# Optimization experiments

Hardware: AMD Instinct MI355X
Metric: run time of the kernel (lower is better)

Reference implementation:

```python
import jax, jax.numpy as jnp
import numpy as np

L, B = 256, 512
K, IN, STATE, OBS = 128, 64, 128, 128


def _preprocess(x, w1, b1, w2, b2):
    # PreProcess: two Linear+ReLU layers mapping raw dim -> k
    t = jax.nn.relu(x @ w1.T + b1)
    return jax.nn.relu(t @ w2.T + b2)


def _dblock_relu(x, w1, b1, w2, b2, wmu, bmu, wls, bls):
    # DBlock (TD-VAE style) with ReLU in place of tanh:
    # t = relu(fc1(x)) * sigmoid(fc2(x)); mu = fc_mu(t); logsigma = fc_logsigma(t)
    t = jax.nn.relu(x @ w1.T + b1) * jax.nn.sigmoid(x @ w2.T + b2)
    return t @ wmu.T + bmu, t @ wls.T + bls


def setup_inputs() -> dict:
    key = jax.random.key(0)
    ks = jax.random.split(key, 24)
    rn = lambda i, shape, s=1.0: jax.random.normal(ks[i], shape, dtype=jnp.float32) * s
    W = 0.05  # small weight scale for numerical stability
    return {
        "external_input_seq": rn(0, (L, B, IN)),
        "observations_seq": rn(1, (L, B, OBS)),
        "eps": rn(2, (L, B, STATE)),
        "u_w1": rn(3, (K, IN), W), "u_b1": jnp.zeros((K,), jnp.float32),
        "u_w2": rn(4, (K, K), W), "u_b2": jnp.zeros((K,), jnp.float32),
        "x_w1": rn(5, (K, OBS), W), "x_b1": jnp.zeros((K,), jnp.float32),
        "x_w2": rn(6, (K, K), W), "x_b2": jnp.zeros((K,), jnp.float32),
        "post_w1": rn(7, (2 * K, 2 * K), W), "post_b1": jnp.zeros((2 * K,), jnp.float32),
        "post_w2": rn(8, (2 * K, 2 * K), W), "post_b2": jnp.zeros((2 * K,), jnp.float32),
        "post_wmu": rn(9, (STATE, 2 * K), W), "post_bmu": jnp.zeros((STATE,), jnp.float32),
        "post_wls": rn(10, (STATE, 2 * K), W), "post_bls": jnp.zeros((STATE,), jnp.float32),
        "gru_wih": rn(11, (3 * K, K), W), "gru_whh": rn(12, (3 * K, K), W),
        "gru_bih": jnp.zeros((3 * K,), jnp.float32), "gru_bhh": jnp.zeros((3 * K,), jnp.float32),
    }


def reference(external_input_seq, observations_seq, eps,
              u_w1, u_b1, u_w2, u_b2,
              x_w1, x_b1, x_w2, x_b2,
              post_w1, post_b1, post_w2, post_b2,
              post_wmu, post_bmu, post_wls, post_bls,
              gru_wih, gru_whh, gru_bih, gru_bhh):
    # _forward_posterior of VAERNN (num_layers=1 GRU)
    u_embed = _preprocess(external_input_seq, u_w1, u_b1, u_w2, u_b2)  # (L,B,K)
    x_embed = _preprocess(observations_seq, x_w1, x_b1, x_w2, x_b2)    # (L,B,K)

    # Precompute input-side GRU gates for all timesteps (one big GEMM)
    x_gates = u_embed @ gru_wih.T + gru_bih  # (L,B,3K)

    h0 = jnp.zeros((external_input_seq.shape[1], K), dtype=external_input_seq.dtype)

    def step(h, xg):
        hg = h @ gru_whh.T + gru_bhh
        xr, xz, xn = jnp.split(xg, 3, axis=-1)
        hr, hz, hn_ = jnp.split(hg, 3, axis=-1)
        r = jax.nn.sigmoid(xr + hr)
        z = jax.nn.sigmoid(xz + hz)
        n = jnp.tanh(xn + r * hn_)
        h_new = (1.0 - z) * n + z * h
        return h_new, h  # emit PRE-update hidden (matches h_seq[:-1])

    hn_final, h_seq = jax.lax.scan(step, h0, x_gates)  # h_seq: (L,B,K)

    # Posterior q(z_t | o_t, h_{t-1}) -- fully parallel over time since z_t
    # never feeds back into the recurrence in this model.
    post_in = jnp.concatenate([x_embed, h_seq], axis=-1)  # (L,B,2K)
    state_mu, state_logsigma = _dblock_relu(
        post_in, post_w1, post_b1, post_w2, post_b2,
        post_wmu, post_bmu, post_wls, post_bls)
    # reparameterized sample from N(mu, diag(exp(logsigma)^2))
    sampled_state = state_mu + jnp.exp(state_logsigma) * eps

    return state_mu, state_logsigma, sampled_state, h_seq, x_embed
```

## Files before the change

kernel.cpp:

```cpp
#include <hip/hip_runtime.h>


typedef __attribute__((ext_vector_type(8))) short bf16x8;
typedef __attribute__((ext_vector_type(4))) short bf16x4;
typedef __attribute__((ext_vector_type(4))) float f32x4;

#define LB 131072

__device__ __forceinline__ short f2b(float f) {
  union { float f; unsigned u; } v; v.f = f;
  unsigned r = (v.u + 0x7FFFu + ((v.u >> 16) & 1u)) >> 16;
  return (short)r;
}
__device__ __forceinline__ float u2f(unsigned u) {
  union { unsigned u; float f; } v; v.u = u << 16; return v.f;
}
__device__ __forceinline__ float rcpf(float x) { return __builtin_amdgcn_rcpf(x); }
__device__ __forceinline__ float exp2f_(float x) { return __builtin_amdgcn_exp2f(x); }
__device__ __forceinline__ float sigm(float x) { return rcpf(1.f + exp2f_(-1.44269504f * x)); }

#define LGKM_BAR()                                          \
  asm volatile("s_waitcnt lgkmcnt(0)" ::: "memory");        \
  __builtin_amdgcn_s_barrier();                             \
  __builtin_amdgcn_sched_barrier(0);

__global__ __launch_bounds__(256) void k_cvt(
    const float* __restrict__ s0, const float* __restrict__ s1,
    const float* __restrict__ s2, const float* __restrict__ s3,
    const float* __restrict__ s4, const float* __restrict__ s5,
    const float* __restrict__ s6, const float* __restrict__ s7,
    const float* __restrict__ s8, const float* __restrict__ s9,
    short* __restrict__ dst)
{
  int i = blockIdx.x * 256 + threadIdx.x;
  if (i >= 352256) return;
  const float* src; int off;
  if      (i <   8192) { src = s0; off = i; }
  else if (i <  24576) { src = s1; off = i - 8192; }
  else if (i <  40960) { src = s2; off = i - 24576; }
  else if (i <  57344) { src = s3; off = i - 40960; }
  else if (i < 106496) { src = s4; off = i - 57344; }
  else if (i < 155648) { src = s5; off = i - 106496; }
  else if (i < 221184) { src = s6; off = i - 155648; }
  else if (i < 286720) { src = s7; off = i - 221184; }
  else if (i < 319488) { src = s8; off = i - 286720; }
  else                 { src = s9; off = i - 319488; }
  dst[i] = f2b(src[off]);
}

#define UT 8
__global__ __launch_bounds__(512) void k_upath(
    const float* __restrict__ x, const short* __restrict__ w1, const float* __restrict__ b1,
    const short* __restrict__ w2, const float* __restrict__ b2,
    const short* __restrict__ wih, const float* __restrict__ bih,
    const float* __restrict__ bhh,
    short* __restrict__ gates)
{
  __shared__ short Xb[32][72];
  __shared__ short Tb[32][136];
  __shared__ short Gb[32][392];
  const int tid = threadIdx.x, w = tid >> 6, l = tid & 63;
  const int lr = l & 15, lg = l >> 4;
  const int n1 = w * 16 + lr;

  bf16x8 wf1[2], wf2[4], wfg[3][4];
  #pragma unroll
  for (int kt = 0; kt < 2; ++kt)
    wf1[kt] = *reinterpret_cast<const bf16x8*>(w1 + (size_t)n1 * 64 + kt * 32 + lg * 8);
  #pragma unroll
  for (int kt = 0; kt < 4; ++kt)
    wf2[kt] = *reinterpret_cast<const bf16x8*>(w2 + (size_t)n1 * 128 + kt * 32 + lg * 8);
  float bgv[3];
  #pragma unroll
  for (int j = 0; j < 3; ++j) {
    const int cg = w * 48 + j * 16 + lr;
    bgv[j] = bih[cg] + (cg < 256 ? bhh[cg] : 0.f);
    #pragma unroll
    for (int kt = 0; kt < 4; ++kt)
      wfg[j][kt] = *reinterpret_cast<const bf16x8*>(wih + (size_t)cg * 128 + kt * 32 + lg * 8);
  }
  const float b1v = b1[n1], b2v = b2[n1];
  const int srow = tid >> 4, scol4 = (tid & 15) * 4, gcol = (tid & 15) * 24;

  float4 sx = *reinterpret_cast<const float4*>(
      x + ((size_t)blockIdx.x * UT * 32 + srow) * 64 + scol4);

  for (int it = 0; it < UT; ++it) {
    const size_t m0 = ((size_t)blockIdx.x * UT + it) * 32;

    {
      bf16x4 p; p[0] = f2b(sx.x); p[1] = f2b(sx.y); p[2] = f2b(sx.z); p[3] = f2b(sx.w);
      *reinterpret_cast<bf16x4*>(&Xb[srow][scol4]) = p;
    }
    LGKM_BAR();

    {
      const size_t mn = ((size_t)blockIdx.x * UT + (it + 1 < UT ? it + 1 : it)) * 32;
      sx = *reinterpret_cast<const float4*>(x + (mn + srow) * 64 + scol4);
    }

    f32x4 a1c[2] = {(f32x4){0.f,0.f,0.f,0.f}, (f32x4){0.f,0.f,0.f,0.f}};
    #pragma unroll
    for (int kt = 0; kt < 2; ++kt) {
      #pragma unroll
      for (int mt = 0; mt < 2; ++mt) {
        bf16x8 af = *reinterpret_cast<const bf16x8*>(&Xb[mt * 16 + lr][kt * 32 + lg * 8]);
        a1c[mt] = __builtin_amdgcn_mfma_f32_16x16x32_bf16(af, wf1[kt], a1c[mt], 0, 0, 0);
      }
    }
    #pragma unroll
    for (int mt = 0; mt < 2; ++mt)
      #pragma unroll
      for (int r = 0; r < 4; ++r) {
        float v = a1c[mt][r] + b1v;
        Tb[mt * 16 + lg * 4 + r][n1] = f2b(v > 0.f ? v : 0.f);
      }
    LGKM_BAR();

    f32x4 a2c[2] = {(f32x4){0.f,0.f,0.f,0.f}, (f32x4){0.f,0.f,0.f,0.f}};
    #pragma unroll
    for (int kt = 0; kt < 4; ++kt) {
      #pragma unroll
      for (int mt = 0; mt < 2; ++mt) {
        bf16x8 af = *reinterpret_cast<const bf16x8*>(&Tb[mt * 16 + lr][kt * 32 + lg * 8]);
        a2c[mt] = __builtin_amdgcn_mfma_f32_16x16x32_bf16(af, wf2[kt], a2c[mt], 0, 0, 0);
      }
    }
    #pragma unroll
    for (int mt = 0; mt < 2; ++mt)
      #pragma unroll
      for (int r = 0; r < 4; ++r) {
        float v = a2c[mt][r] + b2v;
        Gb[mt * 16 + lg * 4 + r][n1] = f2b(v > 0.f ? v : 0.f);
      }
    LGKM_BAR();

    bf16x8 ag[2][4];
    #pragma unroll
    for (int mt = 0; mt < 2; ++mt)
      #pragma unroll
      for (int kt = 0; kt < 4; ++kt)
        ag[mt][kt] = *reinterpret_cast<const bf16x8*>(&Gb[mt * 16 + lr][kt * 32 + lg * 8]);
    LGKM_BAR();

    #pragma unroll
    for (int j = 0; j < 3; ++j) {
      #pragma unroll
      for (int mt = 0; mt < 2; ++mt) {
        f32x4 c = {0.f, 0.f, 0.f, 0.f};
        #pragma unroll
        for (int kt = 0; kt < 4; ++kt)
          c = __builtin_amdgcn_mfma_f32_16x16x32_bf16(ag[mt][kt], wfg[j][kt], c, 0, 0, 0);
        #pragma unroll
        for (int r = 0; r < 4; ++r)
          Gb[mt * 16 + lg * 4 + r][w * 48 + j * 16 + lr] = f2b(c[r] + bgv[j]);
      }
    }
    LGKM_BAR();

    #pragma unroll
    for (int k = 0; k < 3; ++k) {
      bf16x8 vv = *reinterpret_cast<const bf16x8*>(&Gb[srow][gcol + k * 8]);
      *reinterpret_cast<bf16x8*>(gates + (m0 + srow) * 384 + gcol + k * 8) = vv;
    }
  }
}

__global__ __launch_bounds__(512) void k_grux(
    const short* __restrict__ gates, const short* __restrict__ whh,
    const float* __restrict__ bhh, float* __restrict__ hseq,
    const float* __restrict__ obs, const short* __restrict__ xw1,
    const float* __restrict__ xb1, const short* __restrict__ xw2,
    const float* __restrict__ xb2, float* __restrict__ xe)
{
  __shared__ short smem_[41088];
  const int tid = threadIdx.x, w = tid >> 6, l = tid & 63;
  const int lr = l & 15, lg = l >> 4;

  if (blockIdx.x < 128) {
    short (*hb)[16][136] = reinterpret_cast<short (*)[16][136]>(smem_);
    const int m0 = blockIdx.x * 4;
    const int c = w * 16 + lr;
    const int row = lg;
    const size_t gr = m0 + row;

    bf16x8 bfr[3][4];
    #pragma unroll
    for (int g = 0; g < 3; ++g)
      #pragma unroll
      for (int kt = 0; kt < 4; ++kt)
        bfr[g][kt] = *reinterpret_cast<const bf16x8*>(whh + (size_t)(g * 128 + c) * 128 + kt * 32 + lg * 8);
    const float bbn = bhh[256 + c];

    for (int i = tid; i < 2 * 16 * 136; i += 512) smem_[i] = 0;

    float hold = 0.f;

    unsigned gA[3], gB[3];
    #pragma unroll
    for (int g = 0; g < 3; ++g) {
      gA[g] = (unsigned short)gates[gr * 384 + g * 128 + c];
      gB[g] = (unsigned short)gates[(512 + gr) * 384 + g * 128 + c];
    }

    __syncthreads();
    __builtin_amdgcn_s_setprio(1);

#define GATE_E(G, OUT)                                                         \
  {                                                                            \
    f32x4 cc = {0.f, 0.f, 0.f, 0.f};                                           \
    _Pragma("unroll")                                                          \
    for (int kt = 0; kt < 4; ++kt)                                             \
      cc = __builtin_amdgcn_mfma_f32_16x16x32_bf16(a_[kt], bfr[G][kt], cc, 0, 0, 0); \
    unsigned u0 = __float_as_uint(cc[0]), u2 = __float_as_uint(cc[2]);         \
    unsigned u1 = __float_as_uint(cc[1]), u3 = __float_as_uint(cc[3]);         \
    asm volatile("v_permlane32_swap_b32 %0, %1" : "+v"(u0), "+v"(u2));         \
    asm volatile("v_permlane32_swap_b32 %0, %1" : "+v"(u1), "+v"(u3));         \
    asm volatile("v_permlane16_swap_b32 %0, %1" : "+v"(u0), "+v"(u1));         \
    OUT = __uint_as_float(u0);                                                 \
  }

#define GRU_STEP(T, GC, BR, BW)                                                \
  {                                                                            \
    const int t_ = (T);                                                        \
    bf16x8 a_[4];                                                              \
    _Pragma("unroll")                                                          \
    for (int kt = 0; kt < 4; ++kt)                                             \
      a_[kt] = *reinterpret_cast<const bf16x8*>(&hb[BR][lr][kt * 32 + lg * 8]);\
    float e0, e1, e2;                                                          \
    GATE_E(0, e0)                            \
    float rr = sigm(u2f(GC[0]) + e0);                                          \
    GATE_E(2, e2)                                           \
    float tt = u2f(GC[2]) + (e2 + bbn) * rr;                                   \
    float nn = 1.f - 2.f * rcpf(1.f + exp2f_(2.88539008f * tt));               \
    GATE_E(1, e1)                         \
    float zz = sigm(u2f(GC[1]) + e1);                                          \
    float hnew = nn + zz * (hold - nn);                                        \
    hb[BW][row][c] = f2b(hnew);           \
    hseq[((size_t)t_ * 512 + gr) * 128 + c] = hold;                            \
    hold = hnew;                                                               \
    const int tp_ = (t_ + 2) & 255;                                            \
    _Pragma("unroll")                                                          \
    for (int g = 0; g < 3; ++g)                                                \
      GC[g] = (unsigned short)gates[((size_t)tp_ * 512 + gr) * 384 + g * 128 + c]; \
    asm volatile("s_waitcnt lgkmcnt(0)" ::: "memory");                         \
    __builtin_amdgcn_s_barrier();                                              \
    __builtin_amdgcn_sched_barrier(0);                                         \
  }

    for (int tt = 0; tt < 128; ++tt) {
      GRU_STEP(2 * tt,     gA, 0, 1)
      GRU_STEP(2 * tt + 1, gB, 1, 0)
    }
    __builtin_amdgcn_s_setprio(0);
#undef GRU_STEP
#undef GATE_E
  } else {
    const int m0 = (blockIdx.x - 128) * 256 + w * 32;
    short (* __restrict__ B)[136] = reinterpret_cast<short (*)[136]>(&smem_[w * 32 * 136]);

    #pragma unroll
    for (int it = 0; it < 16; ++it) {
      int idx = (it * 64 + l) * 4;
      int row = idx >> 7, col = idx & 127;
      float4 v = *reinterpret_cast<const float4*>(obs + (size_t)(m0 + row) * 128 + col);
      bf16x4 p; p[0] = f2b(v.x); p[1] = f2b(v.y); p[2] = f2b(v.z); p[3] = f2b(v.w);
      *reinterpret_cast<bf16x4*>(&B[row][col]) = p;
    }

    f32x4 acc[2][8];
    bf16x8 a1f[2][4];
    #pragma unroll
    for (int mt = 0; mt < 2; ++mt)
      #pragma unroll
      for (int kt = 0; kt < 4; ++kt)
        a1f[mt][kt] = *reinterpret_cast<const bf16x8*>(&B[mt * 16 + lr][kt * 32 + lg * 8]);
    #pragma unroll
    for (int nt = 0; nt < 8; ++nt)
      #pragma unroll
      for (int mt = 0; mt < 2; ++mt) {
        f32x4 c = {0.f, 0.f, 0.f, 0.f};
        #pragma unroll
        for (int kt = 0; kt < 4; ++kt) {
          bf16x8 bv = *reinterpret_cast<const bf16x8*>(xw1 + (size_t)(nt * 16 + lr) * 128 + kt * 32 + lg * 8);
          c = __builtin_amdgcn_mfma_f32_16x16x32_bf16(a1f[mt][kt], bv, c, 0, 0, 0);
        }
        acc[mt][nt] = c;
      }
    #pragma unroll
    for (int nt = 0; nt < 8; ++nt) {
      float bb = xb1[nt * 16 + lr];
      #pragma unroll
      for (int mt = 0; mt < 2; ++mt)
        #pragma unroll
        for (int r = 0; r < 4; ++r) {
          float v = acc[mt][nt][r] + bb;
          B[mt * 16 + lg * 4 + r][nt * 16 + lr] = f2b(v > 0.f ? v : 0.f);
        }
    }

    bf16x8 a2f[2][4];
    #pragma unroll
    for (int mt = 0; mt < 2; ++mt)
      #pragma unroll
      for (int kt = 0; kt < 4; ++kt)
        a2f[mt][kt] = *reinterpret_cast<const bf16x8*>(&B[mt * 16 + lr][kt * 32 + lg * 8]);
    #pragma unroll
    for (int nt = 0; nt < 8; ++nt) {
      float bb = xb2[nt * 16 + lr];
      #pragma unroll
      for (int mt = 0; mt < 2; ++mt) {
        f32x4 c = {0.f, 0.f, 0.f, 0.f};
        #pragma unroll
        for (int kt = 0; kt < 4; ++kt) {
          bf16x8 bv = *reinterpret_cast<const bf16x8*>(xw2 + (size_t)(nt * 16 + lr) * 128 + kt * 32 + lg * 8);
          c = __builtin_amdgcn_mfma_f32_16x16x32_bf16(a2f[mt][kt], bv, c, 0, 0, 0);
        }
        #pragma unroll
        for (int r = 0; r < 4; ++r) {
          float v = c[r] + bb;
          xe[(size_t)(m0 + mt * 16 + lg * 4 + r) * 128 + nt * 16 + lr] = (v > 0.f ? v : 0.f);
        }
      }
    }
  }
}

#define PT 8
__global__ __launch_bounds__(512) void k_post(
    const float* __restrict__ xe, const float* __restrict__ hs, const float* __restrict__ eps,
    const short* __restrict__ pw1, const float* __restrict__ pb1,
    const short* __restrict__ pw2, const float* __restrict__ pb2,
    const short* __restrict__ pwmu, const float* __restrict__ pbmu,
    const short* __restrict__ pwls, const float* __restrict__ pbls,
    float* __restrict__ mu, float* __restrict__ ls, float* __restrict__ samp)
{
  __shared__ short Ab[32][264];
  const int tid = threadIdx.x, w = tid >> 6, l = tid & 63;
  const int lr = l & 15, lg = l >> 4;
  const int srow = tid >> 4, scol = (tid & 15) * 8;
  const int n2 = w * 16 + lr;

  bf16x8 wf1[2][8];
  float bb1[2], bb2[2];
  #pragma unroll
  for (int j = 0; j < 2; ++j) {
    const int n = w * 32 + j * 16 + lr;
    bb1[j] = pb1[n]; bb2[j] = pb2[n];
    #pragma unroll
    for (int kt = 0; kt < 8; ++kt)
      wf1[j][kt] = *reinterpret_cast<const bf16x8*>(pw1 + (size_t)n * 256 + kt * 32 + lg * 8);
  }
  const float bbm = pbmu[n2], bbl = pbls[n2];

  float4 sx0, sx1, sh0, sh1;
  {
    const size_t m0 = (size_t)blockIdx.x * PT * 32;
    const float* px = xe + (m0 + srow) * 128 + scol;
    sx0 = *reinterpret_cast<const float4*>(px);
    sx1 = *reinterpret_cast<const float4*>(px + 4);
    const float* ph = hs + (m0 + srow) * 128 + scol;
    sh0 = *reinterpret_cast<const float4*>(ph);
    sh1 = *reinterpret_cast<const float4*>(ph + 4);
  }

  for (int it = 0; it < PT; ++it) {
    const size_t m0 = ((size_t)blockIdx.x * PT + it) * 32;

    unsigned long long a2 = (unsigned long long)pw2;
    unsigned long long am_ = (unsigned long long)pwmu;
    unsigned long long al_ = (unsigned long long)pwls;
    asm volatile("" : "+s"(a2), "+s"(am_), "+s"(al_));
    const short* pw2v = (const short*)a2;
    const short* pwmv = (const short*)am_;
    const short* pwlv = (const short*)al_;

    float ev[2][4];
    #pragma unroll
    for (int mt = 0; mt < 2; ++mt)
      #pragma unroll
      for (int r = 0; r < 4; ++r)
        ev[mt][r] = eps[(m0 + mt * 16 + lg * 4 + r) * 128 + n2];

    {
      bf16x8 pk;
      pk[0] = f2b(sx0.x); pk[1] = f2b(sx0.y); pk[2] = f2b(sx0.z); pk[3] = f2b(sx0.w);
      pk[4] = f2b(sx1.x); pk[5] = f2b(sx1.y); pk[6] = f2b(sx1.z); pk[7] = f2b(sx1.w);
      *reinterpret_cast<bf16x8*>(&Ab[srow][scol]) = pk;
      bf16x8 qk;
      qk[0] = f2b(sh0.x); qk[1] = f2b(sh0.y); qk[2] = f2b(sh0.z); qk[3] = f2b(sh0.w);
      qk[4] = f2b(sh1.x); qk[5] = f2b(sh1.y); qk[6] = f2b(sh1.z); qk[7] = f2b(sh1.w);
      *reinterpret_cast<bf16x8*>(&Ab[srow][128 + scol]) = qk;
    }
    LGKM_BAR();

    {
      const size_t mn = ((size_t)blockIdx.x * PT + (it + 1 < PT ? it + 1 : it)) * 32;
      const float* px = xe + (mn + srow) * 128 + scol;
      sx0 = *reinterpret_cast<const float4*>(px);
      sx1 = *reinterpret_cast<const float4*>(px + 4);
      const float* ph = hs + (mn + srow) * 128 + scol;
      sh0 = *reinterpret_cast<const float4*>(ph);
      sh1 = *reinterpret_cast<const float4*>(ph + 4);
    }

    bf16x8 wf2[2][8];
    #pragma unroll
    for (int j = 0; j < 2; ++j) {
      const int n = w * 32 + j * 16 + lr;
      #pragma unroll
      for (int kt = 0; kt < 8; ++kt)
        wf2[j][kt] = *reinterpret_cast<const bf16x8*>(pw2v + (size_t)n * 256 + kt * 32 + lg * 8);
    }
    f32x4 ac1[2][2], ac2[2][2];
    #pragma unroll
    for (int j = 0; j < 2; ++j)
      #pragma unroll
      for (int mt = 0; mt < 2; ++mt) { ac1[j][mt] = (f32x4){0.f,0.f,0.f,0.f}; ac2[j][mt] = (f32x4){0.f,0.f,0.f,0.f}; }
    #pragma unroll
    for (int kt = 0; kt < 8; ++kt) {
      bf16x8 af[2];
      #pragma unroll
      for (int mt = 0; mt < 2; ++mt)
        af[mt] = *reinterpret_cast<const bf16x8*>(&Ab[mt * 16 + lr][kt * 32 + lg * 8]);
      #pragma unroll
      for (int j = 0; j < 2; ++j)
        #pragma unroll
        for (int mt = 0; mt < 2; ++mt) {
          ac1[j][mt] = __builtin_amdgcn_mfma_f32_16x16x32_bf16(af[mt], wf1[j][kt], ac1[j][mt], 0, 0, 0);
          ac2[j][mt] = __builtin_amdgcn_mfma_f32_16x16x32_bf16(af[mt], wf2[j][kt], ac2[j][mt], 0, 0, 0);
        }
    }

    bf16x8 wm[8], wl[8];
    #pragma unroll
    for (int kt = 0; kt < 8; ++kt) {
      wm[kt] = *reinterpret_cast<const bf16x8*>(pwmv + (size_t)n2 * 256 + kt * 32 + lg * 8);
      wl[kt] = *reinterpret_cast<const bf16x8*>(pwlv + (size_t)n2 * 256 + kt * 32 + lg * 8);
    }
    LGKM_BAR();

    #pragma unroll
    for (int j = 0; j < 2; ++j)
      #pragma unroll
      for (int mt = 0; mt < 2; ++mt)
        #pragma unroll
        for (int r = 0; r < 4; ++r) {
          float t1 = ac1[j][mt][r] + bb1[j]; t1 = t1 > 0.f ? t1 : 0.f;
          float t2 = sigm(ac2[j][mt][r] + bb2[j]);
          Ab[mt * 16 + lg * 4 + r][w * 32 + j * 16 + lr] = f2b(t1 * t2);
        }
    LGKM_BAR();

    f32x4 amc[2], alc[2];
    #pragma unroll
    for (int mt = 0; mt < 2; ++mt) { amc[mt] = (f32x4){0.f,0.f,0.f,0.f}; alc[mt] = (f32x4){0.f,0.f,0.f,0.f}; }
    #pragma unroll
    for (int kt = 0; kt < 8; ++kt) {
      bf16x8 at[2];
      #pragma unroll
      for (int mt = 0; mt < 2; ++mt)
        at[mt] = *reinterpret_cast<const bf16x8*>(&Ab[mt * 16 + lr][kt * 32 + lg * 8]);
      #pragma unroll
      for (int mt = 0; mt < 2; ++mt) {
        amc[mt] = __builtin_amdgcn_mfma_f32_16x16x32_bf16(at[mt], wm[kt], amc[mt], 0, 0, 0);
        alc[mt] = __builtin_amdgcn_mfma_f32_16x16x32_bf16(at[mt], wl[kt], alc[mt], 0, 0, 0);
      }
    }
    #pragma unroll
    for (int mt = 0; mt < 2; ++mt)
      #pragma unroll
      for (int r = 0; r < 4; ++r) {
        size_t off = (m0 + mt * 16 + lg * 4 + r) * 128 + n2;
        float m_ = amc[mt][r] + bbm;
        float l_ = alc[mt][r] + bbl;
        mu[off] = m_;
        ls[off] = l_;
        samp[off] = m_ + exp2f_(1.44269504f * l_) * ev[mt][r];
      }
    LGKM_BAR();
  }
}

extern "C" void kernel_launch(void* const* d_in, const int* in_sizes, int n_in,
                              void* d_out, int out_size, void* d_ws, size_t ws_size,
                              hipStream_t stream) {
  const float* ext   = (const float*)d_in[0];
  const float* obs   = (const float*)d_in[1];
  const float* eps   = (const float*)d_in[2];
  const float* u_w1  = (const float*)d_in[3];
  const float* u_b1  = (const float*)d_in[4];
  const float* u_w2  = (const float*)d_in[5];
  const float* u_b2  = (const float*)d_in[6];
  const float* x_w1  = (const float*)d_in[7];
  const float* x_b1  = (const float*)d_in[8];
  const float* x_w2  = (const float*)d_in[9];
  const float* x_b2  = (const float*)d_in[10];
  const float* pw1   = (const float*)d_in[11];
  const float* pb1   = (const float*)d_in[12];
  const float* pw2   = (const float*)d_in[13];
  const float* pb2   = (const float*)d_in[14];
  const float* pwmu  = (const float*)d_in[15];
  const float* pbmu  = (const float*)d_in[16];
  const float* pwls  = (const float*)d_in[17];
  const float* pbls  = (const float*)d_in[18];
  const float* g_wih = (const float*)d_in[19];
  const float* g_whh = (const float*)d_in[20];
  const float* g_bih = (const float*)d_in[21];
  const float* g_bhh = (const float*)d_in[22];

  float* out = (float*)d_out;
  float* o_mu = out;
  float* o_ls = out + 16777216;
  float* o_sp = out + 33554432;
  float* o_hs = out + 50331648;
  float* o_xe = out + 67108864;
  short* gates = (short*)out;

  short* wb = (short*)d_ws;
  short* c_uw1  = wb + 0;
  short* c_uw2  = wb + 8192;
  short* c_xw1  = wb + 24576;
  short* c_xw2  = wb + 40960;
  short* c_wih  = wb + 57344;
  short* c_whh  = wb + 106496;
  short* c_pw1  = wb + 155648;
  short* c_pw2  = wb + 221184;
  short* c_pwmu = wb + 286720;
  short* c_pwls = wb + 319488;

  k_cvt<<<1376, 256, 0, stream>>>(u_w1, u_w2, x_w1, x_w2, g_wih, g_whh,
                                  pw1, pw2, pwmu, pwls, wb);
  k_upath<<<512, 512, 0, stream>>>(ext, c_uw1, u_b1, c_uw2, u_b2, c_wih, g_bih, g_bhh, gates);
  k_grux<<<640, 512, 0, stream>>>(gates, c_whh, g_bhh, o_hs,
                                  obs, c_xw1, x_b1, c_xw2, x_b2, o_xe);
  k_post<<<512, 512, 0, stream>>>(o_xe, o_hs, eps, c_pw1, pb1, c_pw2, pb2,
                                  c_pwmu, pbmu, c_pwls, pbls, o_mu, o_ls, o_sp);
}
```

Baseline: 368.9 us.

## Double per-iteration row tile in posterior kernel to 64 rows

The posterior DBlock kernel now processes 64 rows per iteration instead of 32 and runs half as many iterations per block (PT 8 to 4), so total work per block is unchanged. Each reload of the fc2, mu and logsigma weight fragments from global memory is amortised over twice as many MFMA tiles, and the number of barriers per row drops. In exchange, accumulator and prefetch register pressure roughly doubles, which risks spills or lower occupancy under the 512-thread launch bound, and LDS use doubles.

```diff
diff --git a/kernel.cpp b/kernel.cpp
--- a/kernel.cpp
+++ b/kernel.cpp
@@ -326,7 +326,7 @@
   }
 }
 
-#define PT 8
+#define PT 4
 __global__ __launch_bounds__(512) void k_post(
     const float* __restrict__ xe, const float* __restrict__ hs, const float* __restrict__ eps,
     const short* __restrict__ pw1, const float* __restrict__ pb1,
@@ -335,7 +335,7 @@
     const short* __restrict__ pwls, const float* __restrict__ pbls,
     float* __restrict__ mu, float* __restrict__ ls, float* __restrict__ samp)
 {
-  __shared__ short Ab[32][264];
+  __shared__ short Ab[64][264];
   const int tid = threadIdx.x, w = tid >> 6, l = tid & 63;
   const int lr = l & 15, lg = l >> 4;
   const int srow = tid >> 4, scol = (tid & 15) * 8;
@@ -353,19 +353,22 @@
   }
   const float bbm = pbmu[n2], bbl = pbls[n2];
 
-  float4 sx0, sx1, sh0, sh1;
+  float4 sx0[2], sx1[2], sh0[2], sh1[2];
   {
-    const size_t m0 = (size_t)blockIdx.x * PT * 32;
-    const float* px = xe + (m0 + srow) * 128 + scol;
-    sx0 = *reinterpret_cast<const float4*>(px);
-    sx1 = *reinterpret_cast<const float4*>(px + 4);
-    const float* ph = hs + (m0 + srow) * 128 + scol;
-    sh0 = *reinterpret_cast<const float4*>(ph);
-    sh1 = *reinterpret_cast<const float4*>(ph + 4);
+    const size_t m0 = (size_t)blockIdx.x * PT * 64;
+    #pragma unroll
+    for (int h = 0; h < 2; ++h) {
+      const float* px = xe + (m0 + srow + 32 * h) * 128 + scol;
+      sx0[h] = *reinterpret_cast<const float4*>(px);
+      sx1[h] = *reinterpret_cast<const float4*>(px + 4);
+      const float* ph = hs + (m0 + srow + 32 * h) * 128 + scol;
+      sh0[h] = *reinterpret_cast<const float4*>(ph);
+      sh1[h] = *reinterpret_cast<const float4*>(ph + 4);
+    }
   }
 
   for (int it = 0; it < PT; ++it) {
-    const size_t m0 = ((size_t)blockIdx.x * PT + it) * 32;
+    const size_t m0 = ((size_t)blockIdx.x * PT + it) * 64;
 
     unsigned long long a2 = (unsigned long long)pw2;
     unsigned long long am_ = (unsigned long long)pwmu;
@@ -375,35 +378,40 @@
     const short* pwmv = (const short*)am_;
     const short* pwlv = (const short*)al_;
 
-    float ev[2][4];
-    #pragma unroll
-    for (int mt = 0; mt < 2; ++mt)
+    #pragma unroll
+    for (int h = 0; h < 2; ++h) {
+      const int row = srow + 32 * h;
+      bf16x8 pk;
+      pk[0] = f2b(sx0[h].x); pk[1] = f2b(sx0[h].y); pk[2] = f2b(sx0[h].z); pk[3] = f2b(sx0[h].w);
+      pk[4] = f2b(sx1[h].x); pk[5] = f2b(sx1[h].y); pk[6] = f2b(sx1[h].z); pk[7] = f2b(sx1[h].w);
+      *reinterpret_cast<bf16x8*>(&Ab[row][scol]) = pk;
+      bf16x8 qk;
+      qk[0] = f2b(sh0[h].x); qk[1] = f2b(sh0[h].y); qk[2] = f2b(sh0[h].z); qk[3] = f2b(sh0[h].w);
+      qk[4] = f2b(sh1[h].x); qk[5] = f2b(sh1[h].y); qk[6] = f2b(sh1[h].z); qk[7] = f2b(sh1[h].w);
+      *reinterpret_cast<bf16x8*>(&Ab[row][128 + scol]) = qk;
+    }
+    LGKM_BAR();
+
+    {
+      const size_t mn = ((size_t)blockIdx.x * PT + (it + 1 < PT ? it + 1 : it)) * 64;
+      #pragma unroll
+      for (int h = 0; h < 2; ++h) {
+        const float* px = xe + (mn + srow + 32 * h) * 128 + scol;
+        sx0[h] = *reinterpret_cast<const float4*>(px);
+        sx1[h] = *reinterpret_cast<const float4*>(px + 4);
+        const float* ph = hs + (mn + srow + 32 * h) * 128 + scol;
+        sh0[h] = *reinterpret_cast<const float4*>(ph);
+        sh1[h] = *reinterpret_cast<const float4*>(ph + 4);
+      }
+    }
+
+    float ev[4][4];
+    #pragma unroll
+    for (int mt = 0; mt < 4; ++mt)
       #pragma unroll
       for (int r = 0; r < 4; ++r)
         ev[mt][r] = eps[(m0 + mt * 16 + lg * 4 + r) * 128 + n2];
 
-    {
-      bf16x8 pk;
-      pk[0] = f2b(sx0.x); pk[1] = f2b(sx0.y); pk[2] = f2b(sx0.z); pk[3] = f2b(sx0.w);
-      pk[4] = f2b(sx1.x); pk[5] = f2b(sx1.y); pk[6] = f2b(sx1.z); pk[7] = f2b(sx1.w);
-      *reinterpret_cast<bf16x8*>(&Ab[srow][scol]) = pk;
-      bf16x8 qk;
-      qk[0] = f2b(sh0.x); qk[1] = f2b(sh0.y); qk[2] = f2b(sh0.z); qk[3] = f2b(sh0.w);
-      qk[4] = f2b(sh1.x); qk[5] = f2b(sh1.y); qk[6] = f2b(sh1.z); qk[7] = f2b(sh1.w);
-      *reinterpret_cast<bf16x8*>(&Ab[srow][128 + scol]) = qk;
-    }
-    LGKM_BAR();
-
-    {
-      const size_t mn = ((size_t)blockIdx.x * PT + (it + 1 < PT ? it + 1 : it)) * 32;
-      const float* px = xe + (mn + srow) * 128 + scol;
-      sx0 = *reinterpret_cast<const float4*>(px);
-      sx1 = *reinterpret_cast<const float4*>(px + 4);
-      const float* ph = hs + (mn + srow) * 128 + scol;
-      sh0 = *reinterpret_cast<const float4*>(ph);
-      sh1 = *reinterpret_cast<const float4*>(ph + 4);
-    }
-
     bf16x8 wf2[2][8];
     #pragma unroll
     for (int j = 0; j < 2; ++j) {
@@ -412,21 +420,21 @@
       for (int kt = 0; kt < 8; ++kt)
         wf2[j][kt] = *reinterpret_cast<const bf16x8*>(pw2v + (size_t)n * 256 + kt * 32 + lg * 8);
     }
-    f32x4 ac1[2][2], ac2[2][2];
+    f32x4 ac1[2][4], ac2[2][4];
     #pragma unroll
     for (int j = 0; j < 2; ++j)
       #pragma unroll
-      for (int mt = 0; mt < 2; ++mt) { ac1[j][mt] = (f32x4){0.f,0.f,0.f,0.f}; ac2[j][mt] = (f32x4){0.f,0.f,0.f,0.f}; }
+      for (int mt = 0; mt < 4; ++mt) { ac1[j][mt] = (f32x4){0.f,0.f,0.f,0.f}; ac2[j][mt] = (f32x4){0.f,0.f,0.f,0.f}; }
     #pragma unroll
     for (int kt = 0; kt < 8; ++kt) {
-      bf16x8 af[2];
-      #pragma unroll
-      for (int mt = 0; mt < 2; ++mt)
+      bf16x8 af[4];
+      #pragma unroll
+      for (int mt = 0; mt < 4; ++mt)
         af[mt] = *reinterpret_cast<const bf16x8*>(&Ab[mt * 16 + lr][kt * 32 + lg * 8]);
       #pragma unroll
       for (int j = 0; j < 2; ++j)
         #pragma unroll
-        for (int mt = 0; mt < 2; ++mt) {
+        for (int mt = 0; mt < 4; ++mt) {
           ac1[j][mt] = __builtin_amdgcn_mfma_f32_16x16x32_bf16(af[mt], wf1[j][kt], ac1[j][mt], 0, 0, 0);
           ac2[j][mt] = __builtin_amdgcn_mfma_f32_16x16x32_bf16(af[mt], wf2[j][kt], ac2[j][mt], 0, 0, 0);
         }
@@ -443,7 +451,7 @@
     #pragma unroll
     for (int j = 0; j < 2; ++j)
       #pragma unroll
-      for (int mt = 0; mt < 2; ++mt)
+      for (int mt = 0; mt < 4; ++mt)
         #pragma unroll
         for (int r = 0; r < 4; ++r) {
           float t1 = ac1[j][mt][r] + bb1[j]; t1 = t1 > 0.f ? t1 : 0.f;
@@ -452,23 +460,20 @@
         }
     LGKM_BAR();
 
-    f32x4 amc[2], alc[2];
-    #pragma unroll
-    for (int mt = 0; mt < 2; ++mt) { amc[mt] = (f32x4){0.f,0.f,0.f,0.f}; alc[mt] = (f32x4){0.f,0.f,0.f,0.f}; }
+    f32x4 amc[4], alc[4];
+    #pragma unroll
+    for (int mt = 0; mt < 4; ++mt) { amc[mt] = (f32x4){0.f,0.f,0.f,0.f}; alc[mt] = (f32x4){0.f,0.f,0.f,0.f}; }
     #pragma unroll
     for (int kt = 0; kt < 8; ++kt) {
-      bf16x8 at[2];
-      #pragma unroll
-      for (int mt = 0; mt < 2; ++mt)
-        at[mt] = *reinterpret_cast<const bf16x8*>(&Ab[mt * 16 + lr][kt * 32 + lg * 8]);
-      #pragma unroll
-      for (int mt = 0; mt < 2; ++mt) {
-        amc[mt] = __builtin_amdgcn_mfma_f32_16x16x32_bf16(at[mt], wm[kt], amc[mt], 0, 0, 0);
-        alc[mt] = __builtin_amdgcn_mfma_f32_16x16x32_bf16(at[mt], wl[kt], alc[mt], 0, 0, 0);
-      }
-    }
-    #pragma unroll
-    for (int mt = 0; mt < 2; ++mt)
+      #pragma unroll
+      for (int mt = 0; mt < 4; ++mt) {
+        bf16x8 at = *reinterpret_cast<const bf16x8*>(&Ab[mt * 16 + lr][kt * 32 + lg * 8]);
+        amc[mt] = __builtin_amdgcn_mfma_f32_16x16x32_bf16(at, wm[kt], amc[mt], 0, 0, 0);
+        alc[mt] = __builtin_amdgcn_mfma_f32_16x16x32_bf16(at, wl[kt], alc[mt], 0, 0, 0);
+      }
+    }
+    #pragma unroll
+    for (int mt = 0; mt < 4; ++mt)
       #pragma unroll
       for (int r = 0; r < 4; ++r) {
         size_t off = (m0 + mt * 16 + lg * 4 + r) * 128 + n2;
```

Result: faster. 358.3 us (-2.9%).
